# Kernel optimization log

Measured on AMD Instinct MI355X. Metric: run time of the kernel, lower is better.

## Reference

```python
import jax, jax.numpy as jnp
import numpy as np

N_NODES = 50000
N_DIRECTED = 800000  # symmetrized to 1.6M (src,dst) pairs
IN_FEAT = 256
HEADS = 8
OUT = 64


def setup_inputs() -> dict:
    key = jax.random.key(0)
    k1, k2, k3, k4, k5 = jax.random.split(key, 5)
    r = jax.random.randint(k1, (N_DIRECTED,), 0, N_NODES)
    c = jax.random.randint(k2, (N_DIRECTED,), 0, N_NODES)
    # symmetric adjacency (values = 1), as edge list
    src = jnp.concatenate([r, c])
    dst = jnp.concatenate([c, r])
    x = jax.random.normal(k3, (N_NODES, IN_FEAT), dtype=jnp.float32)
    Ws = jax.random.normal(k4, (HEADS, OUT, IN_FEAT), dtype=jnp.float32) * 0.05
    As = jax.random.normal(k5, (HEADS, 2 * OUT, 1), dtype=jnp.float32) * 0.05
    return {"x": x, "src": src, "dst": dst, "Ws": Ws, "As": As}


def reference(x, src, dst, Ws, As):
    H, O, F = Ws.shape
    N = x.shape[0]
    # t_nodes = inputs @ Ws^T  -> [H, N, O]
    t = jnp.einsum('nf,hof->hno', x, Ws)
    a_l = As[:, :O, 0]   # [H, O]
    a_r = As[:, O:, 0]   # [H, O]
    Al = jnp.einsum('hno,ho->hn', t, a_l)  # [H, N]
    Ar = jnp.einsum('hno,ho->hn', t, a_r)  # [H, N]
    outs = []
    for k in range(H):
        # sparse E[i,j] = Al[i] + Ar[j] on adjacency pattern
        e = Al[k][src] + Ar[k][dst]  # [E]
        # NOTE: original applies tf.sparse.softmax to E directly (its lrelu
        # tensor is computed but never used), so no leaky_relu here.
        m = jax.ops.segment_max(e, src, num_segments=N)
        ex = jnp.exp(e - m[src])
        den = jax.ops.segment_sum(ex, src, num_segments=N)
        alpha = ex / den[src]
        # sparse_dense_matmul(alphas, t_nodes[k])
        h = jax.ops.segment_sum(alpha[:, None] * t[k][dst], src, num_segments=N)
        outs.append(h)
    out = jnp.stack(outs, axis=1)          # [N, H, O]
    out = out.reshape(N, H * O)            # reduction=False -> concat heads
    return jax.nn.elu(out)
```

## Files before the change

### kernel.cpp

```cpp
#include <hip/hip_runtime.h>
#include <hip/hip_bf16.h>

#define NN 50000
#define INF 256
#define NH 8
#define OUTF 64
#define NC 512
#define NGB 3128
#define EPB 8192
#define NBK 391
#define NBX 12501

typedef __attribute__((ext_vector_type(8))) short bf16x8;
typedef __attribute__((ext_vector_type(4))) float f32x4;
typedef __attribute__((ext_vector_type(2))) float v2f;
typedef __attribute__((ext_vector_type(8))) float f32x8;

__device__ __forceinline__ unsigned short f2bf(float f){
  unsigned u = __float_as_uint(f);
  u += 0x7FFFu + ((u>>16)&1u);
  return (unsigned short)(u>>16);
}

__global__ void k_atil(const float* __restrict__ W, const float* __restrict__ As,
                       float* __restrict__ atil, int* __restrict__ cursor){
  const int h = blockIdx.x, f = threadIdx.x;
  if (h==0 && f==0){ cursor[0]=0; cursor[1]=0; }
  float s = 0.f;
  for (int o=0;o<64;o++) s += W[((long)h*64+o)*INF + f] * As[h*128 + 64 + o];
  atil[h*256 + f] = s;
}

__global__ __launch_bounds__(256) void k_front(const float* __restrict__ x,
                                               const float* __restrict__ W,
                                               unsigned short* __restrict__ Wt,
                                               const float* __restrict__ atil,
                                               unsigned short* __restrict__ xb,
                                               float* __restrict__ eAr,
                                               const int* __restrict__ src,
                                               int* __restrict__ M,
                                               int E, int NB){
  __shared__ int hh[NBK];
  const int tid = threadIdx.x;
  const int bid = blockIdx.x;
  if (bid < 8){
    const int r = tid>>2, cb = (tid&3)*64;
    char* tile = (char*)(Wt + (size_t)bid*16384);
    const float* Wr = W + ((long)bid*64 + r)*INF;
#pragma unroll
    for (int i=0;i<16;i++){
      int c = cb + i*4;
      float4 v = *(const float4*)(Wr + c);
      ushort4 b; b.x=f2bf(v.x); b.y=f2bf(v.y); b.z=f2bf(v.z); b.w=f2bf(v.w);
      int addr = r*512 + ((((c>>3) ^ (r&7)))<<4) + ((c&7)<<1);
      *(ushort4*)(tile + addr) = b;
    }
    return;
  }
  if (bid < 8+NB){
    const int b = bid-8;
    for (int i=tid;i<NBK;i+=256) hh[i]=0;
    __syncthreads();
    const int base = b*EPB;
    const int lim = min(E-base, EPB);
    for (int i=tid;i<lim;i+=256) atomicAdd(&hh[src[base+i]>>7], 1);
    __syncthreads();
    for (int i=tid;i<NBK;i+=256) M[(long)i*NB + b] = hh[i];
    return;
  }
  const int w = tid>>6, l = tid&63;
  const long n = (long)(bid-8-NB)*4 + w;
  if (n > NN) return;
  if (n == NN){
    uint2 z; z.x=0; z.y=0;
    *(uint2*)((char*)xb + (size_t)n*512 + l*8) = z;
    if (l < 8) eAr[n*NH + l] = 0.f;
    return;
  }
  float4 v = *(const float4*)(x + n*INF + l*4);
  uint2 d;
  d.x = (unsigned)f2bf(v.x) | ((unsigned)f2bf(v.y)<<16);
  d.y = (unsigned)f2bf(v.z) | ((unsigned)f2bf(v.w)<<16);
  *(uint2*)((char*)xb + (size_t)n*512 + l*8) = d;
  float p[8];
#pragma unroll
  for (int h=0;h<8;h++){
    float4 a = *(const float4*)(atil + h*256 + l*4);
    p[h] = v.x*a.x + v.y*a.y + v.z*a.z + v.w*a.w;
  }
#pragma unroll
  for (int off=1; off<64; off<<=1){
#pragma unroll
    for (int h=0;h<8;h++) p[h] += __shfl_xor(p[h], off, 64);
  }
  if (l < 8){
    float e = p[0];
#pragma unroll
    for (int h=1;h<8;h++) if (l==h) e = p[h];
    eAr[n*NH + l] = __expf(e);
  }
}

__global__ __launch_bounds__(256) void k_bscan(int* __restrict__ M,
                                               int* __restrict__ bOff,
                                               int* __restrict__ bEnd,
                                               int* __restrict__ cursor, int NB){
  __shared__ int lds[256];
  __shared__ int sb;
  const int k = blockIdx.x, tid = threadIdx.x;
  int v = (tid<NB) ? M[(long)k*NB+tid] : 0;
  const int orig = v;
  lds[tid]=v; __syncthreads();
  for (int off=1; off<256; off<<=1){
    int a = (tid>=off)? lds[tid-off] : 0;
    __syncthreads(); lds[tid]+=a; __syncthreads();
  }
  if (tid==255){
    int tot = lds[255];
    int base = atomicAdd(&cursor[0], tot);
    sb = base;
    bOff[k] = base;
    bEnd[k] = base + tot;
  }
  __syncthreads();
  if (tid<NB) M[(long)k*NB+tid] = sb + lds[tid]-orig;
}

__global__ __launch_bounds__(256) void k_bscat(const int* __restrict__ src,
                                               const int* __restrict__ dst,
                                               const int* __restrict__ M,
                                               unsigned* __restrict__ ebuf,
                                               int E, int NB){
  __shared__ int cur[NBK];
  const int tid = threadIdx.x, b = blockIdx.x;
  for (int i=tid;i<NBK;i+=256) cur[i] = M[(long)i*NB + b];
  __syncthreads();
  const int base = b*EPB;
  const int lim = min(E-base, EPB);
  for (int i=tid;i<lim;i+=256){
    int s = src[base+i], d = dst[base+i];
    int p = atomicAdd(&cur[s>>7], 1);
    ebuf[p] = ((unsigned)d<<7) | (unsigned)(s&127);
  }
}

__global__ __launch_bounds__(256) void k_bcnt_final(const unsigned* __restrict__ ebuf,
                                                    const int* __restrict__ bOff,
                                                    const int* __restrict__ bEnd,
                                                    int* __restrict__ rbeg,
                                                    int* __restrict__ rend,
                                                    int* __restrict__ col,
                                                    int* __restrict__ cursor){
  __shared__ int h[128];
  __shared__ int s[128];
  __shared__ int cur[128];
  __shared__ int pend[128];
  __shared__ int sb;
  const int k = blockIdx.x, tid = threadIdx.x;
  if (tid<128) h[tid]=0;
  __syncthreads();
  const int beg = bOff[k], end = bEnd[k];
  for (int i=beg+tid; i<end; i+=256)
    atomicAdd(&h[(int)(ebuf[i] & 127u)], 1);
  __syncthreads();
  int pc = 0;
  if (tid<128){
    pc = (h[tid]+7)&~7;
    s[tid] = pc;
  }
  __syncthreads();
  for (int off=1; off<128; off<<=1){
    int a = (tid>=off && tid<128)? s[tid-off] : 0;
    __syncthreads();
    if (tid<128) s[tid] += a;
    __syncthreads();
  }
  if (tid==0){
    sb = atomicAdd(&cursor[1], s[127]);
  }
  __syncthreads();
  if (tid<128){
    int rp = sb + s[tid] - pc;
    rbeg[(k<<7)+tid] = rp;
    rend[(k<<7)+tid] = rp + pc;
    cur[tid] = rp;
    pend[tid] = rp + pc;
  }
  __syncthreads();
  for (int i=beg+tid; i<end; i+=256){
    unsigned e = ebuf[i];
    int p = atomicAdd(&cur[e & 127u], 1);
    col[p] = (int)(e>>7);
  }
  __syncthreads();
  if (tid<128){
    for (int i=cur[tid]; i<pend[tid]; i++) col[i] = NN;
  }
}

__global__ __launch_bounds__(1024) void k_aggr_gemm(const int* __restrict__ rbeg,
                                                    const int* __restrict__ rend,
                                                    const int* __restrict__ col,
                                                    const unsigned short* __restrict__ xb,
                                                    const float* __restrict__ eAr,
                                                    const unsigned short* __restrict__ Wt,
                                                    float* __restrict__ out){
  __shared__ char gt[16*4096];
  __shared__ float sden[16][8];
  const int tid = threadIdx.x, l = tid&63, wid = tid>>6;
  const long nb = (long)blockIdx.x*16;
  const long l8 = (long)l*8;
  const int lw = l&7;

  {
    const int r = wid;
    const long n = nb + r;
    const int beg = __builtin_amdgcn_readfirstlane(rbeg[n]);
    const int end = __builtin_amdgcn_readfirstlane(rend[n]);
    const char* xbp = (const char*)xb;
    v2f acc[8][2] = {};
    float dnl = 0.f;
    for (int i=beg; i<end; i+=8){
      int cc[8];
#pragma unroll
      for (int e=0;e<8;e++) cc[e] = __builtin_amdgcn_readfirstlane(col[i+e]);
      uint2 q[8];
#pragma unroll
      for (int e=0;e<8;e++) q[e] = *(const uint2*)(xbp + (size_t)cc[e]*512 + l8);
      float wl[8];
#pragma unroll
      for (int e=0;e<8;e++) wl[e] = eAr[(size_t)cc[e]*NH + lw];
#pragma unroll
      for (int e=0;e<8;e++) dnl += wl[e];
#pragma unroll
      for (int e=0;e<8;e++){
        f32x8 wv8 = *(const f32x8*)(eAr + (size_t)cc[e]*NH);
        v2f f01, f23;
        f01.x = __uint_as_float(q[e].x<<16);
        f01.y = __uint_as_float(q[e].x&0xffff0000u);
        f23.x = __uint_as_float(q[e].y<<16);
        f23.y = __uint_as_float(q[e].y&0xffff0000u);
#pragma unroll
        for (int h=0;h<8;h++){
          v2f w2; w2.x = wv8[h]; w2.y = wv8[h];
          acc[h][0] = __builtin_elementwise_fma(w2, f01, acc[h][0]);
          acc[h][1] = __builtin_elementwise_fma(w2, f23, acc[h][1]);
        }
      }
    }
    char* seg = gt + r*4096;
    const int boff = (int)(l8 ^ ((r&7)<<4));
#pragma unroll
    for (int h=0;h<8;h++){
      uint2 d;
      d.x = (unsigned)f2bf(acc[h][0].x) | ((unsigned)f2bf(acc[h][0].y)<<16);
      d.y = (unsigned)f2bf(acc[h][1].x) | ((unsigned)f2bf(acc[h][1].y)<<16);
      *(uint2*)(seg + h*512 + boff) = d;
    }
    if (l<8) sden[r][l] = dnl;
  }
  __syncthreads();

  const int h = wid>>1;
  const int chalf = wid&1;
  const char* Wh = (const char*)Wt + (size_t)h*32768;
  const int row = l&15;
  f32x4 acc2[2] = {};
  for (int ks=0; ks<8; ks++){
    const int ck = ks*4 + (l>>4);
    bf16x8 af = *(const bf16x8*)(gt + row*4096 + h*512 + ((ck ^ (row&7))<<4));
#pragma unroll
    for (int ct=0; ct<2; ct++){
      const int c = chalf*32 + ct*16 + row;
      bf16x8 bfr = *(const bf16x8*)(Wh + c*512 + ((ck ^ (c&7))<<4));
      acc2[ct] = __builtin_amdgcn_mfma_f32_16x16x32_bf16(af, bfr, acc2[ct], 0,0,0);
    }
  }
  float lv[4];
#pragma unroll
  for (int j=0;j<4;j++){
    float dv = sden[(l>>4)*4 + j][h];
    lv[j] = dv>0.f ? 1.f/dv : 0.f;
  }
#pragma unroll
  for (int ct=0; ct<2; ct++){
#pragma unroll
    for (int j=0;j<4;j++){
      long gr = nb + (l>>4)*4 + j;
      if (gr < NN){
        float v = acc2[ct][j] * lv[j];
        out[gr*NC + h*64 + chalf*32 + ct*16 + row] = v>0.f ? v : expm1f(v);
      }
    }
  }
}

extern "C" void kernel_launch(void* const* d_in, const int* in_sizes, int n_in,
                              void* d_out, int out_size, void* d_ws, size_t ws_size,
                              hipStream_t stream){
  const float* x   = (const float*)d_in[0];
  const int*   src = (const int*)d_in[1];
  const int*   dst = (const int*)d_in[2];
  const float* Ws  = (const float*)d_in[3];
  const float* Av  = (const float*)d_in[4];
  const int E = in_sizes[1];
  const int NB = (E + EPB - 1) / EPB;

  char* ws = (char*)d_ws;
  size_t off = 0;
  auto alloc = [&](size_t bytes)->void*{
    void* p = ws + off; off += (bytes + 255) & ~(size_t)255; return p;
  };
  unsigned short* xb   = (unsigned short*)alloc((size_t)50048*512);
  float* eAr           = (float*)alloc((size_t)50048*NH*4);
  float* atil          = (float*)alloc(8*256*4);
  unsigned short* Wt   = (unsigned short*)alloc((size_t)8*32768);
  int*   rbeg          = (int*)alloc(50304*4);
  int*   rend          = (int*)alloc(50304*4);
  int*   M             = (int*)alloc((size_t)NBK*256*4);
  int*   bOff          = (int*)alloc(512*4);
  int*   bEnd          = (int*)alloc(512*4);
  int*   cursor        = (int*)alloc(256);
  int*   col           = (int*)alloc(((size_t)E + 8*50048 + 64)*4);
  unsigned* ebuf       = (unsigned*)alloc((size_t)E*4);

  k_atil<<<8,256,0,stream>>>(Ws, Av, atil, cursor);
  k_front<<<8+NB+NBX,256,0,stream>>>(x, Ws, Wt, atil, xb, eAr, src, M, E, NB);
  k_bscan<<<NBK,256,0,stream>>>(M, bOff, bEnd, cursor, NB);
  k_bscat<<<NB,256,0,stream>>>(src, dst, M, ebuf, E, NB);
  k_bcnt_final<<<NBK,256,0,stream>>>(ebuf, bOff, bEnd, rbeg, rend, col, cursor);
  k_aggr_gemm<<<NGB,1024,0,stream>>>(rbeg, rend, col, xb, eAr, Wt, (float*)d_out);
}
```

Baseline: 287.9 us.

## Sort nodes by degree so aggregation blocks get balanced row lengths

Builds a degree histogram of padded row lengths and counting-sorts node ids into descending-degree order with two new small kernels. The aggregation kernel then processes nodes through this permutation, so the 16 waves in each block have similar edge counts and heavy blocks are scheduled first. The cost being targeted is intra-block imbalance, where a block waits on its slowest row at the barrier before the GEMM stage. In exchange it adds two kernel launches, global atomics, an indirect node lookup, and scattered output row writes.

```diff
diff --git a/kernel.cpp b/kernel.cpp
--- a/kernel.cpp
+++ b/kernel.cpp
@@ -23,9 +23,11 @@
 }
 
 __global__ void k_atil(const float* __restrict__ W, const float* __restrict__ As,
-                       float* __restrict__ atil, int* __restrict__ cursor){
+                       float* __restrict__ atil, int* __restrict__ cursor,
+                       int* __restrict__ dhist){
   const int h = blockIdx.x, f = threadIdx.x;
-  if (h==0 && f==0){ cursor[0]=0; cursor[1]=0; }
+  if (h==0 && f<2) cursor[f]=0;
+  if (h==0) dhist[f]=0;
   float s = 0.f;
   for (int o=0;o<64;o++) s += W[((long)h*64+o)*INF + f] * As[h*128 + 64 + o];
   atil[h*256 + f] = s;
@@ -150,7 +152,8 @@
                                                     int* __restrict__ rbeg,
                                                     int* __restrict__ rend,
                                                     int* __restrict__ col,
-                                                    int* __restrict__ cursor){
+                                                    int* __restrict__ cursor,
+                                                    int* __restrict__ dhist){
   __shared__ int h[128];
   __shared__ int s[128];
   __shared__ int cur[128];
@@ -181,10 +184,15 @@
   __syncthreads();
   if (tid<128){
     int rp = sb + s[tid] - pc;
-    rbeg[(k<<7)+tid] = rp;
-    rend[(k<<7)+tid] = rp + pc;
+    int n = (k<<7)+tid;
+    rbeg[n] = rp;
+    rend[n] = rp + pc;
     cur[tid] = rp;
     pend[tid] = rp + pc;
+    if (n < NN){
+      int b = pc>>3; if (b>255) b=255;
+      atomicAdd(&dhist[255-b], 1);
+    }
   }
   __syncthreads();
   for (int i=beg+tid; i<end; i+=256){
@@ -198,15 +206,45 @@
   }
 }
 
+__global__ __launch_bounds__(256) void k_dscan(const int* __restrict__ dhist,
+                                               int* __restrict__ dcur,
+                                               int* __restrict__ order){
+  __shared__ int lds[256];
+  const int tid = threadIdx.x;
+  int v = dhist[tid];
+  const int orig = v;
+  lds[tid]=v; __syncthreads();
+  for (int off=1; off<256; off<<=1){
+    int a = (tid>=off)? lds[tid-off] : 0;
+    __syncthreads(); lds[tid]+=a; __syncthreads();
+  }
+  dcur[tid] = lds[tid]-orig;
+  if (tid < 48) order[NN + tid] = -1;
+}
+
+__global__ __launch_bounds__(256) void k_dscat(const int* __restrict__ rbeg,
+                                               const int* __restrict__ rend,
+                                               int* __restrict__ dcur,
+                                               int* __restrict__ order){
+  const int n = blockIdx.x*256 + threadIdx.x;
+  if (n >= NN) return;
+  int pc = rend[n] - rbeg[n];
+  int b = pc>>3; if (b>255) b=255;
+  int p = atomicAdd(&dcur[255-b], 1);
+  order[p] = n;
+}
+
 __global__ __launch_bounds__(1024) void k_aggr_gemm(const int* __restrict__ rbeg,
                                                     const int* __restrict__ rend,
                                                     const int* __restrict__ col,
+                                                    const int* __restrict__ order,
                                                     const unsigned short* __restrict__ xb,
                                                     const float* __restrict__ eAr,
                                                     const unsigned short* __restrict__ Wt,
                                                     float* __restrict__ out){
   __shared__ char gt[16*4096];
   __shared__ float sden[16][8];
+  __shared__ int nord[16];
   const int tid = threadIdx.x, l = tid&63, wid = tid>>6;
   const long nb = (long)blockIdx.x*16;
   const long l8 = (long)l*8;
@@ -214,50 +252,53 @@
 
   {
     const int r = wid;
-    const long n = nb + r;
-    const int beg = __builtin_amdgcn_readfirstlane(rbeg[n]);
-    const int end = __builtin_amdgcn_readfirstlane(rend[n]);
-    const char* xbp = (const char*)xb;
-    v2f acc[8][2] = {};
-    float dnl = 0.f;
-    for (int i=beg; i<end; i+=8){
-      int cc[8];
-#pragma unroll
-      for (int e=0;e<8;e++) cc[e] = __builtin_amdgcn_readfirstlane(col[i+e]);
-      uint2 q[8];
-#pragma unroll
-      for (int e=0;e<8;e++) q[e] = *(const uint2*)(xbp + (size_t)cc[e]*512 + l8);
-      float wl[8];
-#pragma unroll
-      for (int e=0;e<8;e++) wl[e] = eAr[(size_t)cc[e]*NH + lw];
-#pragma unroll
-      for (int e=0;e<8;e++) dnl += wl[e];
-#pragma unroll
-      for (int e=0;e<8;e++){
-        f32x8 wv8 = *(const f32x8*)(eAr + (size_t)cc[e]*NH);
-        v2f f01, f23;
-        f01.x = __uint_as_float(q[e].x<<16);
-        f01.y = __uint_as_float(q[e].x&0xffff0000u);
-        f23.x = __uint_as_float(q[e].y<<16);
-        f23.y = __uint_as_float(q[e].y&0xffff0000u);
-#pragma unroll
-        for (int h=0;h<8;h++){
-          v2f w2; w2.x = wv8[h]; w2.y = wv8[h];
-          acc[h][0] = __builtin_elementwise_fma(w2, f01, acc[h][0]);
-          acc[h][1] = __builtin_elementwise_fma(w2, f23, acc[h][1]);
+    const int n = order[nb + r];
+    if (l==0) nord[r] = n;
+    if (n >= 0){
+      const int beg = __builtin_amdgcn_readfirstlane(rbeg[n]);
+      const int end = __builtin_amdgcn_readfirstlane(rend[n]);
+      const char* xbp = (const char*)xb;
+      v2f acc[8][2] = {};
+      float dnl = 0.f;
+      for (int i=beg; i<end; i+=8){
+        int cc[8];
+#pragma unroll
+        for (int e=0;e<8;e++) cc[e] = __builtin_amdgcn_readfirstlane(col[i+e]);
+        uint2 q[8];
+#pragma unroll
+        for (int e=0;e<8;e++) q[e] = *(const uint2*)(xbp + (size_t)cc[e]*512 + l8);
+        float wl[8];
+#pragma unroll
+        for (int e=0;e<8;e++) wl[e] = eAr[(size_t)cc[e]*NH + lw];
+#pragma unroll
+        for (int e=0;e<8;e++) dnl += wl[e];
+#pragma unroll
+        for (int e=0;e<8;e++){
+          f32x8 wv8 = *(const f32x8*)(eAr + (size_t)cc[e]*NH);
+          v2f f01, f23;
+          f01.x = __uint_as_float(q[e].x<<16);
+          f01.y = __uint_as_float(q[e].x&0xffff0000u);
+          f23.x = __uint_as_float(q[e].y<<16);
+          f23.y = __uint_as_float(q[e].y&0xffff0000u);
+#pragma unroll
+          for (int h=0;h<8;h++){
+            v2f w2; w2.x = wv8[h]; w2.y = wv8[h];
+            acc[h][0] = __builtin_elementwise_fma(w2, f01, acc[h][0]);
+            acc[h][1] = __builtin_elementwise_fma(w2, f23, acc[h][1]);
+          }
         }
       }
-    }
-    char* seg = gt + r*4096;
-    const int boff = (int)(l8 ^ ((r&7)<<4));
-#pragma unroll
-    for (int h=0;h<8;h++){
-      uint2 d;
-      d.x = (unsigned)f2bf(acc[h][0].x) | ((unsigned)f2bf(acc[h][0].y)<<16);
-      d.y = (unsigned)f2bf(acc[h][1].x) | ((unsigned)f2bf(acc[h][1].y)<<16);
-      *(uint2*)(seg + h*512 + boff) = d;
-    }
-    if (l<8) sden[r][l] = dnl;
+      char* seg = gt + r*4096;
+      const int boff = (int)(l8 ^ ((r&7)<<4));
+#pragma unroll
+      for (int h=0;h<8;h++){
+        uint2 d;
+        d.x = (unsigned)f2bf(acc[h][0].x) | ((unsigned)f2bf(acc[h][0].y)<<16);
+        d.y = (unsigned)f2bf(acc[h][1].x) | ((unsigned)f2bf(acc[h][1].y)<<16);
+        *(uint2*)(seg + h*512 + boff) = d;
+      }
+      if (l<8) sden[r][l] = dnl;
+    }
   }
   __syncthreads();
 
@@ -277,19 +318,21 @@
     }
   }
   float lv[4];
+  int gn[4];
 #pragma unroll
   for (int j=0;j<4;j++){
-    float dv = sden[(l>>4)*4 + j][h];
+    int rr = (l>>4)*4 + j;
+    gn[j] = nord[rr];
+    float dv = sden[rr][h];
     lv[j] = dv>0.f ? 1.f/dv : 0.f;
   }
 #pragma unroll
   for (int ct=0; ct<2; ct++){
 #pragma unroll
     for (int j=0;j<4;j++){
-      long gr = nb + (l>>4)*4 + j;
-      if (gr < NN){
+      if (gn[j] >= 0){
         float v = acc2[ct][j] * lv[j];
-        out[gr*NC + h*64 + chalf*32 + ct*16 + row] = v>0.f ? v : expm1f(v);
+        out[(long)gn[j]*NC + h*64 + chalf*32 + ct*16 + row] = v>0.f ? v : expm1f(v);
       }
     }
   }
@@ -321,13 +364,18 @@
   int*   bOff          = (int*)alloc(512*4);
   int*   bEnd          = (int*)alloc(512*4);
   int*   cursor        = (int*)alloc(256);
+  int*   dhist         = (int*)alloc(256*4);
+  int*   dcur          = (int*)alloc(256*4);
+  int*   order         = (int*)alloc(50304*4);
   int*   col           = (int*)alloc(((size_t)E + 8*50048 + 64)*4);
   unsigned* ebuf       = (unsigned*)alloc((size_t)E*4);
 
-  k_atil<<<8,256,0,stream>>>(Ws, Av, atil, cursor);
+  k_atil<<<8,256,0,stream>>>(Ws, Av, atil, cursor, dhist);
   k_front<<<8+NB+NBX,256,0,stream>>>(x, Ws, Wt, atil, xb, eAr, src, M, E, NB);
   k_bscan<<<NBK,256,0,stream>>>(M, bOff, bEnd, cursor, NB);
   k_bscat<<<NB,256,0,stream>>>(src, dst, M, ebuf, E, NB);
-  k_bcnt_final<<<NBK,256,0,stream>>>(ebuf, bOff, bEnd, rbeg, rend, col, cursor);
-  k_aggr_gemm<<<NGB,1024,0,stream>>>(rbeg, rend, col, xb, eAr, Wt, (float*)d_out);
-}
+  k_bcnt_final<<<NBK,256,0,stream>>>(ebuf, bOff, bEnd, rbeg, rend, col, cursor, dhist);
+  k_dscan<<<1,256,0,stream>>>(dhist, dcur, order);
+  k_dscat<<<196,256,0,stream>>>(rbeg, rend, dcur, order);
+  k_aggr_gemm<<<NGB,1024,0,stream>>>(rbeg, rend, col, order, xb, eAr, Wt, (float*)d_out);
+}
```

Result: slower. 961.6 us (+234.0%).
